# Optimization experiments

Hardware: AMD Instinct MI355X
Metric: run time of the kernel (lower is better)

Reference implementation:

```python
import jax, jax.numpy as jnp
import numpy as np

# Fixed genome topology (layered DAG, topologically ordered levels)
B = 4096      # batch
N_IN = 512    # input nodes
H1 = 1536     # hidden level 1
H2 = 1536     # hidden level 2
N_OUT = 512   # output nodes
FAN = 32      # fan-in per non-input node


def setup_inputs() -> dict:
    key = jax.random.key(0)
    ks = jax.random.split(key, 10)
    x = jax.random.normal(ks[0], (B, N_IN), dtype=jnp.float32)
    # level 1: sources among inputs [0, N_IN)
    src0 = jax.random.randint(ks[1], (H1 * FAN,), 0, N_IN, dtype=jnp.int32)
    dst0 = jax.random.randint(ks[2], (H1 * FAN,), 0, H1, dtype=jnp.int32)
    w0 = jax.random.normal(ks[3], (H1 * FAN,), dtype=jnp.float32) * 0.1
    # level 2: sources among inputs + level1 [0, N_IN+H1)
    src1 = jax.random.randint(ks[4], (H2 * FAN,), 0, N_IN + H1, dtype=jnp.int32)
    dst1 = jax.random.randint(ks[5], (H2 * FAN,), 0, H2, dtype=jnp.int32)
    w1 = jax.random.normal(ks[6], (H2 * FAN,), dtype=jnp.float32) * 0.1
    # output level: sources among all earlier nodes [0, N_IN+H1+H2)
    src2 = jax.random.randint(ks[7], (N_OUT * FAN,), 0, N_IN + H1 + H2, dtype=jnp.int32)
    dst2 = jax.random.randint(ks[8], (N_OUT * FAN,), 0, N_OUT, dtype=jnp.int32)
    w2 = jax.random.normal(ks[9], (N_OUT * FAN,), dtype=jnp.float32) * 0.1
    return dict(x=x, src0=src0, dst0=dst0, w0=w0,
                src1=src1, dst1=dst1, w1=w1,
                src2=src2, dst2=dst2, w2=w2)


def _level(node_values, src, dst, w, size):
    # per-edge weighted gather: [B, E]
    vals = node_values[:, src] * w
    # scatter-add into destination nodes of this level: [B, size]
    agg = jnp.zeros((node_values.shape[0], size), node_values.dtype).at[:, dst].add(vals)
    # per-node activation (genome.activation == 'relu'); relu(0)=0 matches
    # original's behavior of leaving unconnected nodes at zero
    return jax.nn.relu(agg)


def reference(x, src0, dst0, w0, src1, dst1, w1, src2, dst2, w2):
    nv = x                                        # [B, N_IN]
    h1 = _level(nv, src0, dst0, w0, H1)           # [B, H1]
    nv = jnp.concatenate([nv, h1], axis=1)        # [B, N_IN+H1]
    h2 = _level(nv, src1, dst1, w1, H2)           # [B, H2]
    nv = jnp.concatenate([nv, h2], axis=1)        # [B, N_IN+H1+H2]
    out = _level(nv, src2, dst2, w2, N_OUT)       # [B, N_OUT]
    return out
```

## Files before the change

kernel.cpp:

```cpp
#include <hip/hip_runtime.h>
#include <hip/hip_fp16.h>
#include <stdint.h>

#define BATCH 4096
#define N_IN  512
#define H1    1536
#define H2    1536
#define N_OUT 512
#define FAN   32
#define E0 (H1 * FAN)
#define E1 (H2 * FAN)
#define E2 (N_OUT * FAN)
#define ETOT (E0 + E1 + E2)
#define NNODES (H1 + H2 + N_OUT)
#define MAXDEG 96

#define OFF_EDGES 33554432
#define OFF_CNT   (OFF_EDGES + NNODES * MAXDEG * 8)

__device__ __forceinline__ uint32_t f2bf(float f) {
    uint32_t u = __float_as_uint(f);
    return (u + 0x7fffu + ((u >> 16) & 1u)) >> 16;
}

__global__ __launch_bounds__(256) void k_transpose_in(const float* __restrict__ x,
                                                      uint16_t* __restrict__ xT) {
    __shared__ float tile[32][33];
    const int tx = threadIdx.x, ty = threadIdx.y;
    const int n0 = blockIdx.x * 32;
    const int b0 = blockIdx.y * 32;
#pragma unroll
    for (int k = 0; k < 32; k += 8)
        tile[ty + k][tx] = x[(size_t)(b0 + ty + k) * N_IN + (n0 + tx)];
    __syncthreads();
#pragma unroll
    for (int k = 0; k < 32; k += 8)
        xT[(size_t)(n0 + ty + k) * BATCH + (b0 + tx)] = (uint16_t)f2bf(tile[tx][ty + k]);
}

__global__ __launch_bounds__(256) void k_fill(const int* __restrict__ s0, const int* __restrict__ d0, const float* __restrict__ w0,
                                              const int* __restrict__ s1, const int* __restrict__ d1, const float* __restrict__ w1,
                                              const int* __restrict__ s2, const int* __restrict__ d2, const float* __restrict__ w2,
                                              int* __restrict__ cnt, int2* __restrict__ edges) {
    const int e = blockIdx.x * 256 + threadIdx.x;
    int src, node; float w;
    if (e < E0)           { src = s0[e];          node = d0[e];                w = w0[e]; }
    else if (e < E0 + E1) { int i = e - E0;       src = s1[i]; node = H1 + d1[i];        w = w1[i]; }
    else                  { int i = e - E0 - E1;  src = s2[i]; node = H1 + H2 + d2[i];   w = w2[i]; }
    const int pos = atomicAdd(&cnt[node], 1);
    if (pos < MAXDEG) edges[node * MAXDEG + pos] = make_int2(src, __float_as_int(w));
}

template <bool FP16OUT>
__global__ __launch_bounds__(64)
void k_level(const int2* __restrict__ edges,
             const int* __restrict__ cnt,
             const uint4* __restrict__ nv,
             uint4* __restrict__ outb) {
    __shared__ int2 eds[MAXDEG];
    const int node = blockIdx.y;
    const int tid  = threadIdx.x;
    const int col8 = (blockIdx.x << 6) | tid;

    int c = cnt[node];
    c = (c < 0) ? 0 : (c > MAXDEG ? MAXDEG : c);
    for (int i = tid; i < c; i += 64) eds[i] = edges[node * MAXDEG + i];
    __syncthreads();

    float a0 = 0.f, a1 = 0.f, a2 = 0.f, a3 = 0.f, a4 = 0.f, a5 = 0.f, a6 = 0.f, a7 = 0.f;

#define ACC8(q, W)                                                     \
    a0 = fmaf(__uint_as_float((q).x << 16),          (W), a0);         \
    a1 = fmaf(__uint_as_float((q).x & 0xffff0000u),  (W), a1);         \
    a2 = fmaf(__uint_as_float((q).y << 16),          (W), a2);         \
    a3 = fmaf(__uint_as_float((q).y & 0xffff0000u),  (W), a3);         \
    a4 = fmaf(__uint_as_float((q).z << 16),          (W), a4);         \
    a5 = fmaf(__uint_as_float((q).z & 0xffff0000u),  (W), a5);         \
    a6 = fmaf(__uint_as_float((q).w << 16),          (W), a6);         \
    a7 = fmaf(__uint_as_float((q).w & 0xffff0000u),  (W), a7);

    int j = 0;
    for (; j + 2 <= c; j += 2) {
        const int2 e0 = eds[j];
        const int2 e1 = eds[j + 1];
        const int s0i = __builtin_amdgcn_readfirstlane(e0.x & 4095);
        const int s1i = __builtin_amdgcn_readfirstlane(e1.x & 4095);
        const float wa = __int_as_float(__builtin_amdgcn_readfirstlane(e0.y));
        const float wb = __int_as_float(__builtin_amdgcn_readfirstlane(e1.y));
        const uint4 q0 = nv[((size_t)s0i << 9) | col8];
        const uint4 q1 = nv[((size_t)s1i << 9) | col8];
        ACC8(q0, wa);
        ACC8(q1, wb);
    }
    if (j < c) {
        const int2 e0 = eds[j];
        const int s0i = __builtin_amdgcn_readfirstlane(e0.x & 4095);
        const float wa = __int_as_float(__builtin_amdgcn_readfirstlane(e0.y));
        const uint4 q0 = nv[((size_t)s0i << 9) | col8];
        ACC8(q0, wa);
    }
#undef ACC8

    a0 = fmaxf(a0, 0.f); a1 = fmaxf(a1, 0.f); a2 = fmaxf(a2, 0.f); a3 = fmaxf(a3, 0.f);
    a4 = fmaxf(a4, 0.f); a5 = fmaxf(a5, 0.f); a6 = fmaxf(a6, 0.f); a7 = fmaxf(a7, 0.f);

    uint4 p;
    if (FP16OUT) {
        __half2 h0 = __floats2half2_rn(a0, a1);
        __half2 h1 = __floats2half2_rn(a2, a3);
        __half2 h2 = __floats2half2_rn(a4, a5);
        __half2 h3 = __floats2half2_rn(a6, a7);
        p.x = *(uint32_t*)&h0; p.y = *(uint32_t*)&h1;
        p.z = *(uint32_t*)&h2; p.w = *(uint32_t*)&h3;
    } else {
        p.x = f2bf(a0) | (f2bf(a1) << 16);
        p.y = f2bf(a2) | (f2bf(a3) << 16);
        p.z = f2bf(a4) | (f2bf(a5) << 16);
        p.w = f2bf(a6) | (f2bf(a7) << 16);
    }
    outb[((size_t)node << 9) | col8] = p;
}

__global__ __launch_bounds__(256) void k_transpose_out(const __half* __restrict__ outh,
                                                       float* __restrict__ out) {
    __shared__ float tile[32][33];
    const int tx = threadIdx.x, ty = threadIdx.y;
    const int n0 = blockIdx.x * 32;
    const int b0 = blockIdx.y * 32;
#pragma unroll
    for (int k = 0; k < 32; k += 8)
        tile[ty + k][tx] = __half2float(outh[(size_t)(n0 + ty + k) * BATCH + (b0 + tx)]);
    __syncthreads();
#pragma unroll
    for (int k = 0; k < 32; k += 8)
        out[(size_t)(b0 + ty + k) * N_OUT + (n0 + tx)] = tile[tx][ty + k];
}

extern "C" void kernel_launch(void* const* d_in, const int* in_sizes, int n_in,
                              void* d_out, int out_size, void* d_ws, size_t ws_size,
                              hipStream_t stream) {
    const float* x  = (const float*)d_in[0];
    const int* s0   = (const int*)d_in[1];
    const int* dd0  = (const int*)d_in[2];
    const float* w0 = (const float*)d_in[3];
    const int* s1   = (const int*)d_in[4];
    const int* dd1  = (const int*)d_in[5];
    const float* w1 = (const float*)d_in[6];
    const int* s2   = (const int*)d_in[7];
    const int* dd2  = (const int*)d_in[8];
    const float* w2 = (const float*)d_in[9];

    char* ws        = (char*)d_ws;
    uint4*    nv4   = (uint4*)ws;
    int2*     edges = (int2*)(ws + OFF_EDGES);
    int*      cnt   = (int*)(ws + OFF_CNT);

    hipMemsetAsync(cnt, 0, NNODES * sizeof(int), stream);
    k_fill<<<ETOT / 256, 256, 0, stream>>>(s0, dd0, w0, s1, dd1, w1, s2, dd2, w2, cnt, edges);

    k_transpose_in<<<dim3(N_IN / 32, BATCH / 32), dim3(32, 8), 0, stream>>>(x, (uint16_t*)ws);

    k_level<false><<<dim3(8, H1), 64, 0, stream>>>(edges, cnt, nv4,
                                                   nv4 + (size_t)N_IN * 512);
    k_level<false><<<dim3(8, H2), 64, 0, stream>>>(edges + (size_t)H1 * MAXDEG, cnt + H1, nv4,
                                                   nv4 + (size_t)(N_IN + H1) * 512);
    k_level<true><<<dim3(8, N_OUT), 64, 0, stream>>>(edges + (size_t)(H1 + H2) * MAXDEG, cnt + H1 + H2, nv4,
                                                     nv4 + (size_t)(N_IN + H1 + H2) * 512);

    k_transpose_out<<<dim3(N_OUT / 32, BATCH / 32), dim3(32, 8), 0, stream>>>(
        (const __half*)(ws + (size_t)(N_IN + H1 + H2) * BATCH * 2), (float*)d_out);
}
```

Baseline: 151.1 us.

## Pack four nodes per block, broadcast edges via readlane, store activations in fp16

```diff
diff --git a/kernel.cpp b/kernel.cpp
--- a/kernel.cpp
+++ b/kernel.cpp
@@ -13,18 +13,13 @@
 #define E2 (N_OUT * FAN)
 #define ETOT (E0 + E1 + E2)
 #define NNODES (H1 + H2 + N_OUT)
-#define MAXDEG 96
+#define MAXDEG 128
 
 #define OFF_EDGES 33554432
 #define OFF_CNT   (OFF_EDGES + NNODES * MAXDEG * 8)
 
-__device__ __forceinline__ uint32_t f2bf(float f) {
-    uint32_t u = __float_as_uint(f);
-    return (u + 0x7fffu + ((u >> 16) & 1u)) >> 16;
-}
-
 __global__ __launch_bounds__(256) void k_transpose_in(const float* __restrict__ x,
-                                                      uint16_t* __restrict__ xT) {
+                                                      __half* __restrict__ xT) {
     __shared__ float tile[32][33];
     const int tx = threadIdx.x, ty = threadIdx.y;
     const int n0 = blockIdx.x * 32;
@@ -35,7 +30,7 @@
     __syncthreads();
 #pragma unroll
     for (int k = 0; k < 32; k += 8)
-        xT[(size_t)(n0 + ty + k) * BATCH + (b0 + tx)] = (uint16_t)f2bf(tile[tx][ty + k]);
+        xT[(size_t)(n0 + ty + k) * BATCH + (b0 + tx)] = __float2half_rn(tile[tx][ty + k]);
 }
 
 __global__ __launch_bounds__(256) void k_fill(const int* __restrict__ s0, const int* __restrict__ d0, const float* __restrict__ w0,
@@ -51,73 +46,76 @@
     if (pos < MAXDEG) edges[node * MAXDEG + pos] = make_int2(src, __float_as_int(w));
 }
 
-template <bool FP16OUT>
-__global__ __launch_bounds__(64)
+__global__ __launch_bounds__(256)
 void k_level(const int2* __restrict__ edges,
              const int* __restrict__ cnt,
              const uint4* __restrict__ nv,
              uint4* __restrict__ outb) {
-    __shared__ int2 eds[MAXDEG];
-    const int node = blockIdx.y;
-    const int tid  = threadIdx.x;
-    const int col8 = (blockIdx.x << 6) | tid;
+    const int lane = threadIdx.x & 63;
+    const int wv   = threadIdx.x >> 6;
+    const int node = (blockIdx.y << 2) | wv;
+    const int col8 = (blockIdx.x << 6) | lane;
 
     int c = cnt[node];
     c = (c < 0) ? 0 : (c > MAXDEG ? MAXDEG : c);
-    for (int i = tid; i < c; i += 64) eds[i] = edges[node * MAXDEG + i];
-    __syncthreads();
 
     float a0 = 0.f, a1 = 0.f, a2 = 0.f, a3 = 0.f, a4 = 0.f, a5 = 0.f, a6 = 0.f, a7 = 0.f;
 
-#define ACC8(q, W)                                                     \
-    a0 = fmaf(__uint_as_float((q).x << 16),          (W), a0);         \
-    a1 = fmaf(__uint_as_float((q).x & 0xffff0000u),  (W), a1);         \
-    a2 = fmaf(__uint_as_float((q).y << 16),          (W), a2);         \
-    a3 = fmaf(__uint_as_float((q).y & 0xffff0000u),  (W), a3);         \
-    a4 = fmaf(__uint_as_float((q).z << 16),          (W), a4);         \
-    a5 = fmaf(__uint_as_float((q).z & 0xffff0000u),  (W), a5);         \
-    a6 = fmaf(__uint_as_float((q).w << 16),          (W), a6);         \
-    a7 = fmaf(__uint_as_float((q).w & 0xffff0000u),  (W), a7);
+#define ACC8(q, W) {                                                    \
+    const __half2 h0 = *(const __half2*)&(q).x;                         \
+    const __half2 h1 = *(const __half2*)&(q).y;                         \
+    const __half2 h2 = *(const __half2*)&(q).z;                         \
+    const __half2 h3 = *(const __half2*)&(q).w;                         \
+    a0 = fmaf(__low2float(h0),  (W), a0);                               \
+    a1 = fmaf(__high2float(h0), (W), a1);                               \
+    a2 = fmaf(__low2float(h1),  (W), a2);                               \
+    a3 = fmaf(__high2float(h1), (W), a3);                               \
+    a4 = fmaf(__low2float(h2),  (W), a4);                               \
+    a5 = fmaf(__high2float(h2), (W), a5);                               \
+    a6 = fmaf(__low2float(h3),  (W), a6);                               \
+    a7 = fmaf(__high2float(h3), (W), a7); }
 
-    int j = 0;
-    for (; j + 2 <= c; j += 2) {
-        const int2 e0 = eds[j];
-        const int2 e1 = eds[j + 1];
-        const int s0i = __builtin_amdgcn_readfirstlane(e0.x & 4095);
-        const int s1i = __builtin_amdgcn_readfirstlane(e1.x & 4095);
-        const float wa = __int_as_float(__builtin_amdgcn_readfirstlane(e0.y));
-        const float wb = __int_as_float(__builtin_amdgcn_readfirstlane(e1.y));
-        const uint4 q0 = nv[((size_t)s0i << 9) | col8];
-        const uint4 q1 = nv[((size_t)s1i << 9) | col8];
-        ACC8(q0, wa);
-        ACC8(q1, wb);
-    }
-    if (j < c) {
-        const int2 e0 = eds[j];
-        const int s0i = __builtin_amdgcn_readfirstlane(e0.x & 4095);
-        const float wa = __int_as_float(__builtin_amdgcn_readfirstlane(e0.y));
-        const uint4 q0 = nv[((size_t)s0i << 9) | col8];
-        ACC8(q0, wa);
+    for (int base = 0; base < c; base += 64) {
+        const int2 my = edges[(size_t)node * MAXDEG + base + lane];
+        const int m = (c - base < 64) ? (c - base) : 64;
+        int j = 0;
+        for (; j + 4 <= m; j += 4) {
+            const int   s0i = __builtin_amdgcn_readlane(my.x, j)     & 4095;
+            const int   s1i = __builtin_amdgcn_readlane(my.x, j + 1) & 4095;
+            const int   s2i = __builtin_amdgcn_readlane(my.x, j + 2) & 4095;
+            const int   s3i = __builtin_amdgcn_readlane(my.x, j + 3) & 4095;
+            const float wa  = __int_as_float(__builtin_amdgcn_readlane(my.y, j));
+            const float wb  = __int_as_float(__builtin_amdgcn_readlane(my.y, j + 1));
+            const float wc  = __int_as_float(__builtin_amdgcn_readlane(my.y, j + 2));
+            const float wd  = __int_as_float(__builtin_amdgcn_readlane(my.y, j + 3));
+            const uint4 q0 = nv[((size_t)s0i << 9) | col8];
+            const uint4 q1 = nv[((size_t)s1i << 9) | col8];
+            const uint4 q2 = nv[((size_t)s2i << 9) | col8];
+            const uint4 q3 = nv[((size_t)s3i << 9) | col8];
+            ACC8(q0, wa);
+            ACC8(q1, wb);
+            ACC8(q2, wc);
+            ACC8(q3, wd);
+        }
+        for (; j < m; ++j) {
+            const int   s0i = __builtin_amdgcn_readlane(my.x, j) & 4095;
+            const float wa  = __int_as_float(__builtin_amdgcn_readlane(my.y, j));
+            const uint4 q0 = nv[((size_t)s0i << 9) | col8];
+            ACC8(q0, wa);
+        }
     }
 #undef ACC8
 
     a0 = fmaxf(a0, 0.f); a1 = fmaxf(a1, 0.f); a2 = fmaxf(a2, 0.f); a3 = fmaxf(a3, 0.f);
     a4 = fmaxf(a4, 0.f); a5 = fmaxf(a5, 0.f); a6 = fmaxf(a6, 0.f); a7 = fmaxf(a7, 0.f);
 
+    const __half2 h0 = __floats2half2_rn(a0, a1);
+    const __half2 h1 = __floats2half2_rn(a2, a3);
+    const __half2 h2 = __floats2half2_rn(a4, a5);
+    const __half2 h3 = __floats2half2_rn(a6, a7);
     uint4 p;
-    if (FP16OUT) {
-        __half2 h0 = __floats2half2_rn(a0, a1);
-        __half2 h1 = __floats2half2_rn(a2, a3);
-        __half2 h2 = __floats2half2_rn(a4, a5);
-        __half2 h3 = __floats2half2_rn(a6, a7);
-        p.x = *(uint32_t*)&h0; p.y = *(uint32_t*)&h1;
-        p.z = *(uint32_t*)&h2; p.w = *(uint32_t*)&h3;
-    } else {
-        p.x = f2bf(a0) | (f2bf(a1) << 16);
-        p.y = f2bf(a2) | (f2bf(a3) << 16);
-        p.z = f2bf(a4) | (f2bf(a5) << 16);
-        p.w = f2bf(a6) | (f2bf(a7) << 16);
-    }
+    p.x = *(const uint32_t*)&h0; p.y = *(const uint32_t*)&h1;
+    p.z = *(const uint32_t*)&h2; p.w = *(const uint32_t*)&h3;
     outb[((size_t)node << 9) | col8] = p;
 }
 
@@ -158,14 +156,14 @@
     hipMemsetAsync(cnt, 0, NNODES * sizeof(int), stream);
     k_fill<<<ETOT / 256, 256, 0, stream>>>(s0, dd0, w0, s1, dd1, w1, s2, dd2, w2, cnt, edges);
 
-    k_transpose_in<<<dim3(N_IN / 32, BATCH / 32), dim3(32, 8), 0, stream>>>(x, (uint16_t*)ws);
+    k_transpose_in<<<dim3(N_IN / 32, BATCH / 32), dim3(32, 8), 0, stream>>>(x, (__half*)ws);
 
-    k_level<false><<<dim3(8, H1), 64, 0, stream>>>(edges, cnt, nv4,
-                                                   nv4 + (size_t)N_IN * 512);
-    k_level<false><<<dim3(8, H2), 64, 0, stream>>>(edges + (size_t)H1 * MAXDEG, cnt + H1, nv4,
-                                                   nv4 + (size_t)(N_IN + H1) * 512);
-    k_level<true><<<dim3(8, N_OUT), 64, 0, stream>>>(edges + (size_t)(H1 + H2) * MAXDEG, cnt + H1 + H2, nv4,
-                                                     nv4 + (size_t)(N_IN + H1 + H2) * 512);
+    k_level<<<dim3(8, H1 / 4), 256, 0, stream>>>(edges, cnt, nv4,
+                                                 nv4 + (size_t)N_IN * 512);
+    k_level<<<dim3(8, H2 / 4), 256, 0, stream>>>(edges + (size_t)H1 * MAXDEG, cnt + H1, nv4,
+                                                 nv4 + (size_t)(N_IN + H1) * 512);
+    k_level<<<dim3(8, N_OUT / 4), 256, 0, stream>>>(edges + (size_t)(H1 + H2) * MAXDEG, cnt + H1 + H2, nv4,
+                                                    nv4 + (size_t)(N_IN + H1 + H2) * 512);
 
     k_transpose_out<<<dim3(N_OUT / 32, BATCH / 32), dim3(32, 8), 0, stream>>>(
         (const __half*)(ws + (size_t)(N_IN + H1 + H2) * BATCH * 2), (float*)d_out);
```

Result: faster. 146.9 us (-2.8%).
